# Kernel tuning notes

Hardware: AMD Instinct MI355X
Metric: run time of the kernel (lower is better)

Reference implementation:

```python
import jax, jax.numpy as jnp
import numpy as np

N_NODES = 100000
IN_CH = 128
HID = 128
OUT_CH = 40
K = 3
N_EDGES = 3200000


def setup_inputs() -> dict:
    key = jax.random.key(0)
    ks = jax.random.split(key, 10)
    x = jax.random.normal(ks[0], (N_NODES, IN_CH), dtype=jnp.float32)
    edge_index = jax.random.randint(ks[1], (2, N_EDGES), 0, N_NODES, dtype=jnp.int64)
    s1 = 1.0 / np.sqrt(IN_CH)
    lin1_w = jax.random.uniform(ks[2], (IN_CH, HID), minval=-s1, maxval=s1, dtype=jnp.float32)
    lin1_b = jax.random.uniform(ks[3], (HID,), minval=-s1, maxval=s1, dtype=jnp.float32)
    s2 = 1.0 / np.sqrt(HID)
    gcn_w = jax.random.uniform(ks[4], (K, HID, HID), minval=-s2, maxval=s2, dtype=jnp.float32)
    gcn_b = jnp.zeros((K, HID), dtype=jnp.float32)
    lin2_w = jax.random.uniform(ks[5], (HID, OUT_CH), minval=-s2, maxval=s2, dtype=jnp.float32)
    lin2_b = jax.random.uniform(ks[6], (OUT_CH,), minval=-s2, maxval=s2, dtype=jnp.float32)
    return {"x": x, "edge_index": edge_index, "lin1_w": lin1_w, "lin1_b": lin1_b,
            "gcn_w": gcn_w, "gcn_b": gcn_b, "lin2_w": lin2_w, "lin2_b": lin2_b}


def _gcn_conv(h, w, b, src, dst, norm, n):
    # PyG GCNConv: transform, then symmetric-normalized aggregation (self-loops
    # already included in src/dst/norm), then bias.
    h = h @ w  # [N, H]
    msg = h[src] * norm[:, None]  # [E+N, H] gathered edge messages
    out = jax.ops.segment_sum(msg, dst, num_segments=n)
    return out + b


def reference(x, edge_index, lin1_w, lin1_b, gcn_w, gcn_b, lin2_w, lin2_b):
    n = x.shape[0]
    src, dst = edge_index[0], edge_index[1]
    # add self-loops (GCNConv default add_self_loops=True)
    loop = jnp.arange(n, dtype=src.dtype)
    src = jnp.concatenate([src, loop])
    dst = jnp.concatenate([dst, loop])
    # symmetric normalization D^{-1/2} (A+I) D^{-1/2}
    deg = jax.ops.segment_sum(jnp.ones(src.shape[0], dtype=x.dtype), dst, num_segments=n)
    dinv = jnp.where(deg > 0, jax.lax.rsqrt(deg), 0.0)
    norm = dinv[src] * dinv[dst]  # [E+N]

    h = jax.nn.relu(x @ lin1_w + lin1_b)  # dropout: eval mode (identity)
    for k in range(K):
        h = jax.nn.relu(_gcn_conv(h, gcn_w[k], gcn_b[k], src, dst, norm, n))
    logits = h @ lin2_w + lin2_b
    return jax.nn.log_softmax(logits, axis=1)
```

## Files before the change

### kernel.cpp

```cpp
#include <hip/hip_runtime.h>
#include <math.h>

#define NN 100000
#define NP 100032
#define HIDC 128
#define OUTC 40
#define NBUCK ((NN + 511) >> 9)
#define PT_TILE 8192
#define BCAP 18368

typedef __attribute__((ext_vector_type(2))) float floatx2;
typedef __attribute__((ext_vector_type(4))) float floatx4;
typedef __attribute__((ext_vector_type(8))) short short8;

__device__ __forceinline__ unsigned pack_bf16x2(float a, float b) {
  unsigned ua = __float_as_uint(a), ub = __float_as_uint(b);
  ua = ua + 0x7fff + ((ua >> 16) & 1);
  ub = ub + 0x7fff + ((ub >> 16) & 1);
  return (ua >> 16) | (ub & 0xffff0000u);
}
__device__ __forceinline__ unsigned short bf16r(float x) {
  unsigned u = __float_as_uint(x);
  u = u + 0x7fff + ((u >> 16) & 1);
  return (unsigned short)(u >> 16);
}


__global__ __launch_bounds__(256) void partition_kernel(
    const int* __restrict__ src, const int* __restrict__ dst,
    int* __restrict__ bcur, unsigned* __restrict__ pairs, int E) {
  __shared__ int hist[256];
  __shared__ int base[256];
  __shared__ int lcur[256];
  int t = threadIdx.x;
  hist[t] = 0; lcur[t] = 0;
  __syncthreads();
  int e0 = blockIdx.x * PT_TILE;
  int ec = E - e0; if (ec > PT_TILE) ec = PT_TILE;
  for (int i = t; i < ec; i += 256)
    atomicAdd(&hist[dst[e0 + i] >> 9], 1);
  __syncthreads();
  if (hist[t] > 0) base[t] = atomicAdd(&bcur[t], hist[t]);
  __syncthreads();
  for (int i = t; i < ec; i += 256) {
    int d = dst[e0 + i], s = src[e0 + i];
    int b = d >> 9;
    int pos = atomicAdd(&lcur[b], 1);
    pairs[base[b] + pos] = ((unsigned)(d & 511) << 17) | (unsigned)s;
  }
}

__global__ __launch_bounds__(256) void bucket_fill_kernel(
    const unsigned* __restrict__ pairs, const int* __restrict__ bcur,
    float* __restrict__ dinv, int* __restrict__ csr,
    int* __restrict__ sbeg, int* __restrict__ send,
    float* __restrict__ sdinv, int* __restrict__ sdn, int N) {
  int b = blockIdx.x;
  int d0 = b << 9;
  int nd = N - d0; if (nd > 512) nd = 512;
  __shared__ int hist[512];
  __shared__ int cur[512];
  __shared__ int sums[256];
  int t = threadIdx.x;
  hist[t] = 0; hist[t + 256] = 0;
  __syncthreads();
  int rbeg = b * BCAP, rend = bcur[b];
  for (int i = rbeg + t; i < rend; i += 256)
    atomicAdd(&hist[pairs[i] >> 17], 1);
  __syncthreads();
  int h0 = hist[2 * t], h1 = hist[2 * t + 1];
  int s = h0 + h1;
  sums[t] = s;
  __syncthreads();
  for (int off = 1; off < 256; off <<= 1) {
    int u = (t >= off) ? sums[t - off] : 0;
    __syncthreads();
    sums[t] += u;
    __syncthreads();
  }
  int base0 = rbeg + sums[t] - s;
  int base1 = base0 + h0;
  int j0 = 2 * t, j1 = 2 * t + 1;
  float di0 = rsqrtf((float)(h0 + 1));
  float di1 = rsqrtf((float)(h1 + 1));
  if (j0 < nd) { dinv[d0 + j0] = di0; cur[j0] = base0; }
  if (j1 < nd) { dinv[d0 + j1] = di1; cur[j1] = base1; }
  __syncthreads();

  if (t < 128) hist[t] = 0;
  __syncthreads();
  int c0 = h0 < 127 ? h0 : 127;
  int c1 = h1 < 127 ? h1 : 127;
  if (j0 < nd) atomicAdd(&hist[c0], 1);
  if (j1 < nd) atomicAdd(&hist[c1], 1);
  __syncthreads();
  int dv = (t < 128) ? hist[t] : 0;
  sums[t] = dv;
  __syncthreads();
  for (int off = 1; off < 128; off <<= 1) {
    int u = (t >= off) ? sums[t - off] : 0;
    __syncthreads();
    sums[t] += u;
    __syncthreads();
  }
  if (t < 128) hist[128 + t] = sums[t] - dv;
  __syncthreads();
  if (j0 < nd) {
    int pos = d0 + atomicAdd(&hist[128 + c0], 1);
    sbeg[pos] = base0; send[pos] = base0 + h0; sdinv[pos] = di0; sdn[pos] = d0 + j0;
  }
  if (j1 < nd) {
    int pos = d0 + atomicAdd(&hist[128 + c1], 1);
    sbeg[pos] = base1; send[pos] = base1 + h1; sdinv[pos] = di1; sdn[pos] = d0 + j1;
  }
  __syncthreads();

  for (int i = rbeg + t; i < rend; i += 256) {
    unsigned pk = pairs[i];
    int q = atomicAdd(&cur[pk >> 17], 1);
    csr[q] = pk & 0x1FFFF;
  }
}


__global__ __launch_bounds__(256) void prep_misc_kernel(
    const float* __restrict__ lin1_w, const float* __restrict__ gcn_w,
    const float* __restrict__ lin2_w, int* __restrict__ bcur,
    unsigned short* __restrict__ Wt, unsigned short* __restrict__ W2t) {
  int b = blockIdx.x;
  int t = threadIdx.x;
  if (b == 0) {
    if (t < NBUCK) bcur[t] = t * BCAP;
  } else if (b <= 4) {
    const float* src = (b == 1) ? lin1_w : (gcn_w + (size_t)(b - 2) * 16384);
    unsigned short* dst = Wt + (size_t)(b - 1) * 16384;
    for (int i = t; i < 16384; i += 256) {
      int n = i >> 7, k = i & 127;
      dst[(size_t)n * 128 + k] = bf16r(src[(size_t)k * 128 + n]);
    }
  } else {
    for (int i = t; i < 48 * 128; i += 256) {
      int n = i >> 7, k = i & 127;
      W2t[i] = (n < OUTC) ? bf16r(lin2_w[(size_t)k * OUTC + n]) : (unsigned short)0;
    }
  }
}


template <int MODE>
__global__ __launch_bounds__(256) void gemm_mfma_kernel(
    const void* __restrict__ Av, const unsigned short* __restrict__ Wt,
    const float* __restrict__ bias, const float* __restrict__ dinv,
    void* __restrict__ Y, int M) {
  int t = threadIdx.x;
  int w = t >> 6;
  int l = t & 63;
  int quad = l >> 4;
  int m16 = l & 15;
  int row0 = blockIdx.x * 64;
  int colbase = w * 32;

  floatx4 acc[4][2];
#pragma unroll
  for (int rt = 0; rt < 4; rt++)
#pragma unroll
    for (int ct = 0; ct < 2; ct++) acc[rt][ct] = (floatx4)0.f;

#pragma unroll
  for (int kc = 0; kc < 4; kc++) {
    int kof = kc * 32 + quad * 8;
    short8 a0 = *(const short8*)(Wt + (size_t)(colbase + m16) * 128 + kof);
    short8 a1 = *(const short8*)(Wt + (size_t)(colbase + 16 + m16) * 128 + kof);
#pragma unroll
    for (int rt = 0; rt < 4; rt++) {
      short8 bfr;
      if (MODE == 2) {
        const float* Af = (const float*)Av + (size_t)(row0 + rt * 16 + m16) * 128 + kof;
        float4 f0 = *(const float4*)Af;
        float4 f1 = *(const float4*)(Af + 4);
        unsigned u0 = pack_bf16x2(f0.x, f0.y);
        unsigned u1 = pack_bf16x2(f0.z, f0.w);
        unsigned u2 = pack_bf16x2(f1.x, f1.y);
        unsigned u3 = pack_bf16x2(f1.z, f1.w);
        bfr[0] = (short)(u0 & 0xFFFF); bfr[1] = (short)(u0 >> 16);
        bfr[2] = (short)(u1 & 0xFFFF); bfr[3] = (short)(u1 >> 16);
        bfr[4] = (short)(u2 & 0xFFFF); bfr[5] = (short)(u2 >> 16);
        bfr[6] = (short)(u3 & 0xFFFF); bfr[7] = (short)(u3 >> 16);
      } else {
        bfr = *(const short8*)((const unsigned short*)Av +
                               (size_t)(row0 + rt * 16 + m16) * 128 + kof);
      }
      acc[rt][0] = __builtin_amdgcn_mfma_f32_16x16x32_bf16(a0, bfr, acc[rt][0], 0, 0, 0);
      acc[rt][1] = __builtin_amdgcn_mfma_f32_16x16x32_bf16(a1, bfr, acc[rt][1], 0, 0, 0);
    }
  }

  if (MODE != 1) {
    unsigned short* Y16 = (unsigned short*)Y;
    float4 bv0 = *(const float4*)(bias + colbase + quad * 4);
    float4 bv1 = *(const float4*)(bias + colbase + 16 + quad * 4);
#pragma unroll
    for (int rt = 0; rt < 4; rt++) {
      int row = row0 + rt * 16 + m16;
      if (row < M) {
        uint2 s0, s1;
        s0.x = pack_bf16x2(fmaxf(acc[rt][0][0] + bv0.x, 0.f),
                           fmaxf(acc[rt][0][1] + bv0.y, 0.f));
        s0.y = pack_bf16x2(fmaxf(acc[rt][0][2] + bv0.z, 0.f),
                           fmaxf(acc[rt][0][3] + bv0.w, 0.f));
        s1.x = pack_bf16x2(fmaxf(acc[rt][1][0] + bv1.x, 0.f),
                           fmaxf(acc[rt][1][1] + bv1.y, 0.f));
        s1.y = pack_bf16x2(fmaxf(acc[rt][1][2] + bv1.z, 0.f),
                           fmaxf(acc[rt][1][3] + bv1.w, 0.f));
        *(uint2*)(Y16 + (size_t)row * 128 + colbase + quad * 4) = s0;
        *(uint2*)(Y16 + (size_t)row * 128 + colbase + 16 + quad * 4) = s1;
      }
    }
  } else {
    unsigned* Y8 = (unsigned*)Y;
#pragma unroll
    for (int rt = 0; rt < 4; rt++) {
      int row = row0 + rt * 16 + m16;
      if (row < M) {
        float dd = dinv[row];
        unsigned u0 = 0, u1 = 0;
        u0 = __builtin_amdgcn_cvt_pk_fp8_f32(acc[rt][0][0] * dd, acc[rt][0][1] * dd, (int)u0, false);
        u0 = __builtin_amdgcn_cvt_pk_fp8_f32(acc[rt][0][2] * dd, acc[rt][0][3] * dd, (int)u0, true);
        u1 = __builtin_amdgcn_cvt_pk_fp8_f32(acc[rt][1][0] * dd, acc[rt][1][1] * dd, (int)u1, false);
        u1 = __builtin_amdgcn_cvt_pk_fp8_f32(acc[rt][1][2] * dd, acc[rt][1][3] * dd, (int)u1, true);
        Y8[(size_t)row * 32 + (colbase >> 2) + quad] = u0;
        Y8[(size_t)row * 32 + ((colbase + 16) >> 2) + quad] = u1;
      }
    }
  }
}


#define ACC8(u)                                                       \
  acc[0] += __builtin_amdgcn_cvt_pk_f32_fp8((int)(u).x, false);       \
  acc[1] += __builtin_amdgcn_cvt_pk_f32_fp8((int)(u).x, true);        \
  acc[2] += __builtin_amdgcn_cvt_pk_f32_fp8((int)(u).y, false);       \
  acc[3] += __builtin_amdgcn_cvt_pk_f32_fp8((int)(u).y, true);        \
  acc[4] += __builtin_amdgcn_cvt_pk_f32_fp8((int)(u).z, false);       \
  acc[5] += __builtin_amdgcn_cvt_pk_f32_fp8((int)(u).z, true);        \
  acc[6] += __builtin_amdgcn_cvt_pk_f32_fp8((int)(u).w, false);       \
  acc[7] += __builtin_amdgcn_cvt_pk_f32_fp8((int)(u).w, true);

__global__ __launch_bounds__(256) void aggregate_fp8_kernel(
    const uint4* __restrict__ Ht8, const int* __restrict__ csr,
    const int* __restrict__ sbeg, const int* __restrict__ send,
    const float* __restrict__ sdinv, const int* __restrict__ sdn,
    const float* __restrict__ bias, uint4* __restrict__ Out, int N) {
  int wid = (blockIdx.x * blockDim.x + threadIdx.x) >> 6;
  int lane = threadIdx.x & 63;
  int g = lane >> 3;
  int c8 = lane & 7;
  int idx = wid * 8 + g;
  if (idx >= N) return;
  int beg = sbeg[idx], end = send[idx];
  int d = sdn[idx];

  floatx2 acc[8];
  {
    uint4 us = Ht8[(size_t)d * 8 + c8];
    acc[0] = __builtin_amdgcn_cvt_pk_f32_fp8((int)us.x, false);
    acc[1] = __builtin_amdgcn_cvt_pk_f32_fp8((int)us.x, true);
    acc[2] = __builtin_amdgcn_cvt_pk_f32_fp8((int)us.y, false);
    acc[3] = __builtin_amdgcn_cvt_pk_f32_fp8((int)us.y, true);
    acc[4] = __builtin_amdgcn_cvt_pk_f32_fp8((int)us.z, false);
    acc[5] = __builtin_amdgcn_cvt_pk_f32_fp8((int)us.z, true);
    acc[6] = __builtin_amdgcn_cvt_pk_f32_fp8((int)us.w, false);
    acc[7] = __builtin_amdgcn_cvt_pk_f32_fp8((int)us.w, true);
  }
  int i = beg;
  for (; i + 1 < end; i += 2) {
    int s0 = csr[i], s1 = csr[i + 1];
    uint4 u0 = Ht8[(size_t)s0 * 8 + c8];
    uint4 u1 = Ht8[(size_t)s1 * 8 + c8];
    ACC8(u0) ACC8(u1)
  }
  if (i < end) {
    uint4 u0 = Ht8[(size_t)csr[i] * 8 + c8];
    ACC8(u0)
  }

  float dd = sdinv[idx];
  const float4* b4 = (const float4*)bias;
  float4 bv0 = b4[4 * c8 + 0];
  float4 bv1 = b4[4 * c8 + 1];
  float4 bv2 = b4[4 * c8 + 2];
  float4 bv3 = b4[4 * c8 + 3];
  uint4 o0, o1;
  o0.x = pack_bf16x2(fmaxf(fmaf(dd, acc[0][0], bv0.x), 0.f),
                     fmaxf(fmaf(dd, acc[0][1], bv0.y), 0.f));
  o0.y = pack_bf16x2(fmaxf(fmaf(dd, acc[1][0], bv0.z), 0.f),
                     fmaxf(fmaf(dd, acc[1][1], bv0.w), 0.f));
  o0.z = pack_bf16x2(fmaxf(fmaf(dd, acc[2][0], bv1.x), 0.f),
                     fmaxf(fmaf(dd, acc[2][1], bv1.y), 0.f));
  o0.w = pack_bf16x2(fmaxf(fmaf(dd, acc[3][0], bv1.z), 0.f),
                     fmaxf(fmaf(dd, acc[3][1], bv1.w), 0.f));
  o1.x = pack_bf16x2(fmaxf(fmaf(dd, acc[4][0], bv2.x), 0.f),
                     fmaxf(fmaf(dd, acc[4][1], bv2.y), 0.f));
  o1.y = pack_bf16x2(fmaxf(fmaf(dd, acc[5][0], bv2.z), 0.f),
                     fmaxf(fmaf(dd, acc[5][1], bv2.w), 0.f));
  o1.z = pack_bf16x2(fmaxf(fmaf(dd, acc[6][0], bv3.x), 0.f),
                     fmaxf(fmaf(dd, acc[6][1], bv3.y), 0.f));
  o1.w = pack_bf16x2(fmaxf(fmaf(dd, acc[7][0], bv3.z), 0.f),
                     fmaxf(fmaf(dd, acc[7][1], bv3.w), 0.f));
  Out[(size_t)d * 16 + 2 * c8] = o0;
  Out[(size_t)d * 16 + 2 * c8 + 1] = o1;
}


__global__ __launch_bounds__(256) void head_mfma_kernel(
    const unsigned short* __restrict__ A, const unsigned short* __restrict__ W2t,
    const float* __restrict__ b2, float* __restrict__ Out, int N) {
  __shared__ float lg[64][48];
  __shared__ float bs[48];
  int t = threadIdx.x;
  int w = t >> 6, l = t & 63, quad = l >> 4, m16 = l & 15;
  if (t < 48) bs[t] = (t < OUTC) ? b2[t] : 0.f;
  int row0 = blockIdx.x * 64;

  floatx4 acc[3];
  acc[0] = (floatx4)0.f; acc[1] = (floatx4)0.f; acc[2] = (floatx4)0.f;
  const unsigned short* Aw = A + (size_t)(row0 + w * 16) * 128;
#pragma unroll
  for (int kc = 0; kc < 4; kc++) {
    int kof = kc * 32 + quad * 8;
    short8 a = *(const short8*)(Aw + (size_t)m16 * 128 + kof);
#pragma unroll
    for (int ct = 0; ct < 3; ct++) {
      short8 b = *(const short8*)(W2t + (size_t)(ct * 16 + m16) * 128 + kof);
      acc[ct] = __builtin_amdgcn_mfma_f32_16x16x32_bf16(a, b, acc[ct], 0, 0, 0);
    }
  }
#pragma unroll
  for (int ct = 0; ct < 3; ct++)
#pragma unroll
    for (int j = 0; j < 4; j++)
      lg[w * 16 + quad * 4 + j][ct * 16 + m16] = acc[ct][j];
  __syncthreads();

  int r = t >> 2, sub = t & 3;
  int row = row0 + r;
  float vals[10];
  float mx = -3.4e38f;
#pragma unroll
  for (int j = 0; j < 10; j++) {
    float v = lg[r][sub * 10 + j] + bs[sub * 10 + j];
    vals[j] = v;
    mx = fmaxf(mx, v);
  }
  mx = fmaxf(mx, __shfl_xor(mx, 1, 64));
  mx = fmaxf(mx, __shfl_xor(mx, 2, 64));
  float se = 0.f;
#pragma unroll
  for (int j = 0; j < 10; j++) se += expf(vals[j] - mx);
  se += __shfl_xor(se, 1, 64);
  se += __shfl_xor(se, 2, 64);
  if (row < N) {
    float ls = logf(se);
#pragma unroll
    for (int j = 0; j < 10; j++)
      Out[(size_t)row * OUTC + sub * 10 + j] = vals[j] - mx - ls;
  }
}


extern "C" void kernel_launch(void* const* d_in, const int* in_sizes, int n_in,
                              void* d_out, int out_size, void* d_ws, size_t ws_size,
                              hipStream_t stream) {
  const float* x      = (const float*)d_in[0];
  const int*   edge   = (const int*)d_in[1];
  const float* lin1_w = (const float*)d_in[2];
  const float* lin1_b = (const float*)d_in[3];
  const float* gcn_w  = (const float*)d_in[4];
  const float* gcn_b  = (const float*)d_in[5];
  const float* lin2_w = (const float*)d_in[6];
  const float* lin2_b = (const float*)d_in[7];
  float* out = (float*)d_out;

  const int N = NN;
  const int E = in_sizes[1] / 2;
  const int* src = edge;
  const int* dst = edge + E;

  char* p = (char*)d_ws;
  auto alloc = [&](size_t bytes) { char* q = p; p += (bytes + 255) & ~(size_t)255; return q; };
  unsigned*       hA16    = (unsigned*)alloc((size_t)NP * 128 * 2);
  unsigned*       hB8     = (unsigned*)alloc((size_t)NP * 32 * 4);
  unsigned*       pairs   = (unsigned*)alloc((size_t)NBUCK * BCAP * 4);
  int*            csr     = (int*)alloc((size_t)NBUCK * BCAP * 4);
  float*          dinv    = (float*)alloc((size_t)NP * 4);
  int*            sbeg    = (int*)alloc((size_t)N * 4);
  int*            send    = (int*)alloc((size_t)N * 4);
  float*          sdinv   = (float*)alloc((size_t)N * 4);
  int*            sdn     = (int*)alloc((size_t)N * 4);
  unsigned short* Wt      = (unsigned short*)alloc((size_t)4 * 16384 * 2);
  unsigned short* W2t     = (unsigned short*)alloc((size_t)48 * 128 * 2);
  int*            bcur    = (int*)alloc(256 * 4);

  prep_misc_kernel<<<6, 256, 0, stream>>>(lin1_w, gcn_w, lin2_w, bcur, Wt, W2t);
  partition_kernel<<<(E + PT_TILE - 1) / PT_TILE, 256, 0, stream>>>(src, dst, bcur, pairs, E);
  bucket_fill_kernel<<<NBUCK, 256, 0, stream>>>(pairs, bcur, dinv, csr,
                                                sbeg, send, sdinv, sdn, N);

  int gb = NP / 64;
  gemm_mfma_kernel<2><<<gb, 256, 0, stream>>>((const void*)x, Wt,
                                              lin1_b, nullptr, (void*)hA16, N);
  int ablocks = (N / 8 + 3) / 4;
  for (int k = 0; k < 3; k++) {
    gemm_mfma_kernel<1><<<gb, 256, 0, stream>>>((const void*)hA16,
                                                Wt + (size_t)(k + 1) * 16384,
                                                nullptr, dinv, (void*)hB8, N);
    aggregate_fp8_kernel<<<ablocks, 256, 0, stream>>>(
        (const uint4*)hB8, csr, sbeg, send, sdinv, sdn, gcn_b + (size_t)k * 128,
        (uint4*)hA16, N);
  }
  head_mfma_kernel<<<gb, 256, 0, stream>>>((const unsigned short*)hA16, W2t,
                                           lin2_b, out, N);
}
```

Before: 535.5 us.

## Widen bucket fill, split weight prep, unroll aggregation by four, shrink blocks

Several independent tweaks. The partition tile is halved to launch more blocks, and bucket_fill now runs with 1024 threads, one node per thread over a 512-wide scan. Weight transposition is split across 35 blocks instead of 6. The aggregation loop is unrolled by four to keep more gathers in flight, and its blocks shrink to 128 threads. These aim to raise parallelism and memory-level parallelism in the graph-preprocessing and gather phases, at the cost of more barriers in the wider scan and higher register pressure in aggregation.

```diff
diff --git a/kernel.cpp b/kernel.cpp
--- a/kernel.cpp
+++ b/kernel.cpp
@@ -6,7 +6,7 @@
 #define HIDC 128
 #define OUTC 40
 #define NBUCK ((NN + 511) >> 9)
-#define PT_TILE 8192
+#define PT_TILE 4096
 #define BCAP 18368
 
 typedef __attribute__((ext_vector_type(2))) float floatx2;
@@ -50,7 +50,7 @@
   }
 }
 
-__global__ __launch_bounds__(256) void bucket_fill_kernel(
+__global__ __launch_bounds__(1024) void bucket_fill_kernel(
     const unsigned* __restrict__ pairs, const int* __restrict__ bcur,
     float* __restrict__ dinv, int* __restrict__ csr,
     int* __restrict__ sbeg, int* __restrict__ send,
@@ -60,62 +60,54 @@
   int nd = N - d0; if (nd > 512) nd = 512;
   __shared__ int hist[512];
   __shared__ int cur[512];
-  __shared__ int sums[256];
+  __shared__ int sums[512];
   int t = threadIdx.x;
-  hist[t] = 0; hist[t + 256] = 0;
+  if (t < 512) hist[t] = 0;
   __syncthreads();
   int rbeg = b * BCAP, rend = bcur[b];
-  for (int i = rbeg + t; i < rend; i += 256)
+  for (int i = rbeg + t; i < rend; i += 1024)
     atomicAdd(&hist[pairs[i] >> 17], 1);
   __syncthreads();
-  int h0 = hist[2 * t], h1 = hist[2 * t + 1];
-  int s = h0 + h1;
-  sums[t] = s;
-  __syncthreads();
-  for (int off = 1; off < 256; off <<= 1) {
-    int u = (t >= off) ? sums[t - off] : 0;
+  int h = 0;
+  if (t < 512) { h = hist[t]; sums[t] = h; }
+  __syncthreads();
+  for (int off = 1; off < 512; off <<= 1) {
+    int u = (t < 512 && t >= off) ? sums[t - off] : 0;
     __syncthreads();
-    sums[t] += u;
+    if (t < 512) sums[t] += u;
     __syncthreads();
   }
-  int base0 = rbeg + sums[t] - s;
-  int base1 = base0 + h0;
-  int j0 = 2 * t, j1 = 2 * t + 1;
-  float di0 = rsqrtf((float)(h0 + 1));
-  float di1 = rsqrtf((float)(h1 + 1));
-  if (j0 < nd) { dinv[d0 + j0] = di0; cur[j0] = base0; }
-  if (j1 < nd) { dinv[d0 + j1] = di1; cur[j1] = base1; }
+  int base = 0; float di = 0.f;
+  if (t < 512) {
+    base = rbeg + sums[t] - h;
+    di = rsqrtf((float)(h + 1));
+    if (t < nd) { dinv[d0 + t] = di; cur[t] = base; }
+  }
   __syncthreads();
 
   if (t < 128) hist[t] = 0;
   __syncthreads();
-  int c0 = h0 < 127 ? h0 : 127;
-  int c1 = h1 < 127 ? h1 : 127;
-  if (j0 < nd) atomicAdd(&hist[c0], 1);
-  if (j1 < nd) atomicAdd(&hist[c1], 1);
+  int c = h < 127 ? h : 127;
+  if (t < nd) atomicAdd(&hist[c], 1);
   __syncthreads();
   int dv = (t < 128) ? hist[t] : 0;
-  sums[t] = dv;
+  if (t < 128) sums[t] = dv;
   __syncthreads();
   for (int off = 1; off < 128; off <<= 1) {
-    int u = (t >= off) ? sums[t - off] : 0;
+    int u = (t < 128 && t >= off) ? sums[t - off] : 0;
     __syncthreads();
-    sums[t] += u;
+    if (t < 128) sums[t] += u;
     __syncthreads();
   }
   if (t < 128) hist[128 + t] = sums[t] - dv;
   __syncthreads();
-  if (j0 < nd) {
-    int pos = d0 + atomicAdd(&hist[128 + c0], 1);
-    sbeg[pos] = base0; send[pos] = base0 + h0; sdinv[pos] = di0; sdn[pos] = d0 + j0;
-  }
-  if (j1 < nd) {
-    int pos = d0 + atomicAdd(&hist[128 + c1], 1);
-    sbeg[pos] = base1; send[pos] = base1 + h1; sdinv[pos] = di1; sdn[pos] = d0 + j1;
-  }
-  __syncthreads();
-
-  for (int i = rbeg + t; i < rend; i += 256) {
+  if (t < nd) {
+    int pos = d0 + atomicAdd(&hist[128 + c], 1);
+    sbeg[pos] = base; send[pos] = base + h; sdinv[pos] = di; sdn[pos] = d0 + t;
+  }
+  __syncthreads();
+
+  for (int i = rbeg + t; i < rend; i += 1024) {
     unsigned pk = pairs[i];
     int q = atomicAdd(&cur[pk >> 17], 1);
     csr[q] = pk & 0x1FFFF;
@@ -131,15 +123,20 @@
   int t = threadIdx.x;
   if (b == 0) {
     if (t < NBUCK) bcur[t] = t * BCAP;
-  } else if (b <= 4) {
-    const float* src = (b == 1) ? lin1_w : (gcn_w + (size_t)(b - 2) * 16384);
-    unsigned short* dst = Wt + (size_t)(b - 1) * 16384;
-    for (int i = t; i < 16384; i += 256) {
+  } else if (b <= 32) {
+    int m = (b - 1) >> 3;
+    int chunk = (b - 1) & 7;
+    const float* src = (m == 0) ? lin1_w : (gcn_w + (size_t)(m - 1) * 16384);
+    unsigned short* dstp = Wt + (size_t)m * 16384;
+    int i0 = chunk * 2048;
+    for (int i = i0 + t; i < i0 + 2048; i += 256) {
       int n = i >> 7, k = i & 127;
-      dst[(size_t)n * 128 + k] = bf16r(src[(size_t)k * 128 + n]);
+      dstp[(size_t)n * 128 + k] = bf16r(src[(size_t)k * 128 + n]);
     }
   } else {
-    for (int i = t; i < 48 * 128; i += 256) {
+    int chunk = b - 33;
+    int i0 = chunk * 3072;
+    for (int i = i0 + t; i < i0 + 3072; i += 256) {
       int n = i >> 7, k = i & 127;
       W2t[i] = (n < OUTC) ? bf16r(lin2_w[(size_t)k * OUTC + n]) : (unsigned short)0;
     }
@@ -246,7 +243,7 @@
   acc[6] += __builtin_amdgcn_cvt_pk_f32_fp8((int)(u).w, false);       \
   acc[7] += __builtin_amdgcn_cvt_pk_f32_fp8((int)(u).w, true);
 
-__global__ __launch_bounds__(256) void aggregate_fp8_kernel(
+__global__ __launch_bounds__(128) void aggregate_fp8_kernel(
     const uint4* __restrict__ Ht8, const int* __restrict__ csr,
     const int* __restrict__ sbeg, const int* __restrict__ send,
     const float* __restrict__ sdinv, const int* __restrict__ sdn,
@@ -273,11 +270,20 @@
     acc[7] = __builtin_amdgcn_cvt_pk_f32_fp8((int)us.w, true);
   }
   int i = beg;
-  for (; i + 1 < end; i += 2) {
+  for (; i + 3 < end; i += 4) {
+    int s0 = csr[i], s1 = csr[i + 1], s2 = csr[i + 2], s3 = csr[i + 3];
+    uint4 u0 = Ht8[(size_t)s0 * 8 + c8];
+    uint4 u1 = Ht8[(size_t)s1 * 8 + c8];
+    uint4 u2 = Ht8[(size_t)s2 * 8 + c8];
+    uint4 u3 = Ht8[(size_t)s3 * 8 + c8];
+    ACC8(u0) ACC8(u1) ACC8(u2) ACC8(u3)
+  }
+  if (i + 1 < end) {
     int s0 = csr[i], s1 = csr[i + 1];
     uint4 u0 = Ht8[(size_t)s0 * 8 + c8];
     uint4 u1 = Ht8[(size_t)s1 * 8 + c8];
     ACC8(u0) ACC8(u1)
+    i += 2;
   }
   if (i < end) {
     uint4 u0 = Ht8[(size_t)csr[i] * 8 + c8];
@@ -401,20 +407,20 @@
   unsigned short* W2t     = (unsigned short*)alloc((size_t)48 * 128 * 2);
   int*            bcur    = (int*)alloc(256 * 4);
 
-  prep_misc_kernel<<<6, 256, 0, stream>>>(lin1_w, gcn_w, lin2_w, bcur, Wt, W2t);
+  prep_misc_kernel<<<35, 256, 0, stream>>>(lin1_w, gcn_w, lin2_w, bcur, Wt, W2t);
   partition_kernel<<<(E + PT_TILE - 1) / PT_TILE, 256, 0, stream>>>(src, dst, bcur, pairs, E);
-  bucket_fill_kernel<<<NBUCK, 256, 0, stream>>>(pairs, bcur, dinv, csr,
-                                                sbeg, send, sdinv, sdn, N);
+  bucket_fill_kernel<<<NBUCK, 1024, 0, stream>>>(pairs, bcur, dinv, csr,
+                                                 sbeg, send, sdinv, sdn, N);
 
   int gb = NP / 64;
   gemm_mfma_kernel<2><<<gb, 256, 0, stream>>>((const void*)x, Wt,
                                               lin1_b, nullptr, (void*)hA16, N);
-  int ablocks = (N / 8 + 3) / 4;
+  int ablocks = (N / 8 + 1) / 2;
   for (int k = 0; k < 3; k++) {
     gemm_mfma_kernel<1><<<gb, 256, 0, stream>>>((const void*)hA16,
                                                 Wt + (size_t)(k + 1) * 16384,
                                                 nullptr, dinv, (void*)hB8, N);
-    aggregate_fp8_kernel<<<ablocks, 256, 0, stream>>>(
+    aggregate_fp8_kernel<<<ablocks, 128, 0, stream>>>(
         (const uint4*)hB8, csr, sbeg, send, sdinv, sdn, gcn_b + (size_t)k * 128,
         (uint4*)hA16, N);
   }
```

After: 506.8 us. 1.06x faster.
